# Optimization experiments

Hardware: AMD Instinct MI355X
Metric: run time of the kernel (lower is better)

Reference implementation:

```python
import jax, jax.numpy as jnp
import numpy as np
from jax import lax

N, C, S_CH = 16, 256, 512  # batch, content channels (c_in=c_out), style channels
DN = ('NCHW', 'OIHW', 'NCHW')


def setup_inputs() -> dict:
    key = jax.random.key(0)
    ks = jax.random.split(key, 8)
    p = lambda k, s: jax.random.normal(k, s, jnp.float32) * 0.05
    return {
        'style_encoding': jax.random.normal(ks[0], (N, S_CH, 4, 4), jnp.float32),
        'content_in': jax.random.normal(ks[1], (N, C, 64, 64), jnp.float32),
        # depthwise_kernel_conv: Conv2d(512, n_groups=1, kernel=2)
        'dw_w': p(ks[2], (1, S_CH, 2, 2)), 'dw_b': p(ks[3], (1,)),
        # pw_cn_kn: Conv2d(512, pointwise_groups=1, 1)
        'pw_kn_w': p(ks[4], (1, S_CH, 1, 1)), 'pw_kn_b': p(ks[5], (1,)),
        # pw_cn_bias: Conv2d(512, c_out=256, 1)
        'pw_bias_w': p(ks[6], (C, S_CH, 1, 1)), 'pw_bias_b': p(ks[7], (C,)),
    }


def reference(style_encoding, content_in, dw_w, dw_b, pw_kn_w, pw_kn_b, pw_bias_w, pw_bias_b):
    n = style_encoding.shape[0]
    # depthwise kernel prediction: (N,1,3,3) -> expand -> (N, c_out, c_in, 3, 3)
    dk = lax.conv_general_dilated(style_encoding, dw_w, (1, 1), 'VALID',
                                  dimension_numbers=DN) + dw_b[None, :, None, None]
    depthwise = jnp.broadcast_to(dk[:, None], (n, C, C, 3, 3))
    # AvgPool2d(4) on 4x4 spatial == global mean -> (N,512,1,1)
    s_d = jnp.mean(style_encoding, axis=(2, 3))  # (N,512)
    # 1x1 convs on 1x1 spatial are plain matmuls
    pw1 = s_d @ pw_kn_w[:, :, 0, 0].T + pw_kn_b              # (N,1)
    pointwise_kn = jnp.broadcast_to(pw1[:, None, :, None, None], (n, C, C, 1, 1))
    pointwise_bias = s_d @ pw_bias_w[:, :, 0, 0].T + pw_bias_b  # (N,256)
    # ReflectionPad2d((1,1,1,1))
    x = jnp.pad(content_in, ((0, 0), (0, 0), (1, 1), (1, 1)), mode='reflect')

    def sample_conv(xi, wi, pwi, bi):
        # xi: (C,H+2,W+2), wi: (C,C,3,3) dynamic per-sample weight (groups=1)
        d = lax.conv_general_dilated(xi[None], wi, (1, 1), 'VALID',
                                     dimension_numbers=DN)[0]  # (C,H,W)
        # pointwise 1x1 conv with per-sample weight + bias
        return jnp.einsum('oi,ihw->ohw', pwi[:, :, 0, 0], d) + bi[:, None, None]

    return jax.vmap(sample_conv)(x, depthwise, pointwise_kn, pointwise_bias)
```

## Files before the change

### kernel.cpp

```cpp
#include <hip/hip_runtime.h>


#define OFF_SCALE 0
#define OFF_K     16
#define OFF_SD    160
#define OFF_XP    8352

__global__ __launch_bounds__(256, 2) void ada_front(
    const float* __restrict__ style,
    const float* __restrict__ content,
    const float* __restrict__ dw_w,
    const float* __restrict__ dw_b,
    const float* __restrict__ pw_kn_w,
    const float* __restrict__ pw_kn_b,
    float* __restrict__ ws)
{
    const int t = threadIdx.x;
    __shared__ float red[4][10];

    if (blockIdx.x >= 16) {
        const int b  = blockIdx.x - 16;
        const int n  = b >> 5;
        const int g  = (b >> 2) & 7;
        const int pt = b & 3;
        const int p4 = pt * 256 + t;

        const float4* src = (const float4*)content
                          + ((size_t)(n * 256 + g * 32)) * 1024 + p4;
        float4 a = make_float4(0.f, 0.f, 0.f, 0.f);
#pragma unroll 8
        for (int c = 0; c < 32; ++c) {
            float4 v = src[(size_t)c * 1024];
            a.x += v.x; a.y += v.y; a.z += v.z; a.w += v.w;
        }
        ((float4*)(ws + OFF_XP))[((size_t)(n * 8 + g)) * 1024 + p4] = a;
        return;
    }

    const int n = blockIdx.x;

    float acc[10];
#pragma unroll
    for (int j = 0; j < 10; ++j) acc[j] = 0.f;

#pragma unroll
    for (int cc = 0; cc < 2; ++cc) {
        const int c = t + cc * 256;
        const float4* sp = (const float4*)(style + ((size_t)n * 512 + c) * 16);
        float v[16];
#pragma unroll
        for (int q = 0; q < 4; ++q) {
            float4 f = sp[q];
            v[q*4+0] = f.x; v[q*4+1] = f.y; v[q*4+2] = f.z; v[q*4+3] = f.w;
        }
        float sum = 0.f;
#pragma unroll
        for (int q = 0; q < 16; ++q) sum += v[q];
        const float sdc = sum * 0.0625f;
        ws[OFF_SD + n * 512 + c] = sdc;

        const float* w = dw_w + c * 4;
        const float w00 = w[0], w01 = w[1], w10 = w[2], w11 = w[3];
#pragma unroll
        for (int ki = 0; ki < 3; ++ki)
#pragma unroll
            for (int kj = 0; kj < 3; ++kj)
                acc[ki*3+kj] += v[ki*4 + kj]       * w00
                              + v[ki*4 + kj + 1]   * w01
                              + v[(ki+1)*4 + kj]   * w10
                              + v[(ki+1)*4 + kj+1] * w11;
        acc[9] += sdc * pw_kn_w[c];
    }

#pragma unroll
    for (int off = 32; off >= 1; off >>= 1)
#pragma unroll
        for (int j = 0; j < 10; ++j)
            acc[j] += __shfl_down(acc[j], off, 64);

    if ((t & 63) == 0) {
#pragma unroll
        for (int j = 0; j < 10; ++j) red[t >> 6][j] = acc[j];
    }
    __syncthreads();

    if (t < 10) {
        const float s = red[0][t] + red[1][t] + red[2][t] + red[3][t];
        if (t < 9) ws[OFF_K + n * 9 + t] = s + dw_b[0];
        else       ws[OFF_SCALE + n]     = 256.f * (s + pw_kn_b[0]);
    }
}

__global__ __launch_bounds__(256, 2) void ada_back(
    const float* __restrict__ ws,
    const float* __restrict__ pw_bias_w,
    const float* __restrict__ pw_bias_b,
    float4* __restrict__ out)
{
    const int bid = blockIdx.x;
    const int n   = bid >> 6;
    const int s   = bid & 63;
    const int t   = threadIdx.x;

    __shared__ float Xs[4096];
    __shared__ float bias_s[4];

    {
        const int wv = t >> 6, l = t & 63;
        const int o  = s * 4 + wv;
        const float4* wr = (const float4*)(pw_bias_w + (size_t)o * 512);
        const float4* sv = (const float4*)(ws + OFF_SD + (size_t)n * 512);
        const float4 a0 = wr[l * 2],     a1 = wr[l * 2 + 1];
        const float4 s0 = sv[l * 2],     s1 = sv[l * 2 + 1];
        float d = a0.x*s0.x + a0.y*s0.y + a0.z*s0.z + a0.w*s0.w
                + a1.x*s1.x + a1.y*s1.y + a1.z*s1.z + a1.w*s1.w;
#pragma unroll
        for (int off = 32; off >= 1; off >>= 1)
            d += __shfl_down(d, off, 64);
        if (l == 0) bias_s[wv] = d + pw_bias_b[o];
    }

    const float4* Xp = (const float4*)(ws + OFF_XP) + (size_t)n * 8 * 1024;
#pragma unroll
    for (int i = 0; i < 4; ++i) {
        const int p4 = i * 256 + t;
        float4 a = Xp[p4];
#pragma unroll
        for (int g = 1; g < 8; ++g) {
            float4 v = Xp[g * 1024 + p4];
            a.x += v.x; a.y += v.y; a.z += v.z; a.w += v.w;
        }
        ((float4*)Xs)[p4] = a;
    }

    float k[9];
#pragma unroll
    for (int j = 0; j < 9; ++j) k[j] = ws[OFF_K + n * 9 + j];
    const float scale = ws[OFF_SCALE + n];
    __syncthreads();

    const float b0 = bias_s[0], b1 = bias_s[1], b2 = bias_s[2], b3 = bias_s[3];
    float4* obase = out + ((size_t)(n * 256 + s * 4)) * 1024;

#pragma unroll
    for (int q = 0; q < 4; ++q) {
        const int h  = q * 16 + (t >> 4);
        const int w0 = (t & 15) * 4;
        const int hm = (h == 0)  ? 1  : h - 1;
        const int hp = (h == 63) ? 62 : h + 1;
        float e0 = 0.f, e1 = 0.f, e2 = 0.f, e3 = 0.f;
        const int rows[3] = { hm, h, hp };
#pragma unroll
        for (int i = 0; i < 3; ++i) {
            const float* R = &Xs[rows[i] * 64];
            const float4 m    = *(const float4*)&R[w0];
            const float  left  = (w0 == 0)  ? R[1]  : R[w0 - 1];
            const float  right = (w0 == 60) ? R[62] : R[w0 + 4];
            const float k0 = k[i*3], k1 = k[i*3+1], k2 = k[i*3+2];
            e0 += k0*left + k1*m.x + k2*m.y;
            e1 += k0*m.x  + k1*m.y + k2*m.z;
            e2 += k0*m.y  + k1*m.z + k2*m.w;
            e3 += k0*m.z  + k1*m.w + k2*right;
        }
        e0 *= scale; e1 *= scale; e2 *= scale; e3 *= scale;

        float4* o = obase + q * 256 + t;
        o[0]    = make_float4(e0 + b0, e1 + b0, e2 + b0, e3 + b0);
        o[1024] = make_float4(e0 + b1, e1 + b1, e2 + b1, e3 + b1);
        o[2048] = make_float4(e0 + b2, e1 + b2, e2 + b2, e3 + b2);
        o[3072] = make_float4(e0 + b3, e1 + b3, e2 + b3, e3 + b3);
    }
}

extern "C" void kernel_launch(void* const* d_in, const int* in_sizes, int n_in,
                              void* d_out, int out_size, void* d_ws, size_t ws_size,
                              hipStream_t stream)
{
    const float* style     = (const float*)d_in[0];
    const float* content   = (const float*)d_in[1];
    const float* dw_w      = (const float*)d_in[2];
    const float* dw_b      = (const float*)d_in[3];
    const float* pw_kn_w   = (const float*)d_in[4];
    const float* pw_kn_b   = (const float*)d_in[5];
    const float* pw_bias_w = (const float*)d_in[6];
    const float* pw_bias_b = (const float*)d_in[7];
    float*  ws  = (float*)d_ws;
    float4* out = (float4*)d_out;

    ada_front<<<16 + 512, 256, 0, stream>>>(style, content, dw_w, dw_b,
                                            pw_kn_w, pw_kn_b, ws);
    ada_back <<<1024,     256, 0, stream>>>(ws, pw_bias_w, pw_bias_b, out);
}
```

Before: 31.03 us.

## Reduce all channel partials in front kernel via shared memory instead of back kernel

The front kernel's content-sum blocks now each cover a 32-float4 pixel slice across all 8 channel groups. They combine the 8 partial sums with a shared-memory tree reduction and write one fully reduced channel-sum per pixel. The back kernel then loads a single summed plane instead of reading and adding 8 partial planes in each of its 1024 blocks. This removes 8x redundant workspace reads per sample (64 blocks per sample each reread them). The cost is narrower per-block memory access (32 float4 per row segment) and extra barriers in the front kernel.

```diff
diff --git a/kernel.cpp b/kernel.cpp
--- a/kernel.cpp
+++ b/kernel.cpp
@@ -4,7 +4,7 @@
 #define OFF_SCALE 0
 #define OFF_K     16
 #define OFF_SD    160
-#define OFF_XP    8352
+#define OFF_XS    8352
 
 __global__ __launch_bounds__(256, 2) void ada_front(
     const float* __restrict__ style,
@@ -17,23 +17,40 @@
 {
     const int t = threadIdx.x;
     __shared__ float red[4][10];
+    __shared__ float4 part[8][32];
 
     if (blockIdx.x >= 16) {
-        const int b  = blockIdx.x - 16;
-        const int n  = b >> 5;
-        const int g  = (b >> 2) & 7;
-        const int pt = b & 3;
-        const int p4 = pt * 256 + t;
+        const int b   = blockIdx.x - 16;
+        const int n   = b >> 5;
+        const int sl  = b & 31;
+        const int col = t & 31;
+        const int g   = t >> 5;
 
         const float4* src = (const float4*)content
-                          + ((size_t)(n * 256 + g * 32)) * 1024 + p4;
+                          + ((size_t)(n * 256 + g * 32)) * 1024 + sl * 32 + col;
         float4 a = make_float4(0.f, 0.f, 0.f, 0.f);
 #pragma unroll 8
         for (int c = 0; c < 32; ++c) {
             float4 v = src[(size_t)c * 1024];
             a.x += v.x; a.y += v.y; a.z += v.z; a.w += v.w;
         }
-        ((float4*)(ws + OFF_XP))[((size_t)(n * 8 + g)) * 1024 + p4] = a;
+        part[g][col] = a;
+        __syncthreads();
+        if (g < 4) {
+            float4 v = part[g + 4][col], u = part[g][col];
+            part[g][col] = make_float4(u.x + v.x, u.y + v.y, u.z + v.z, u.w + v.w);
+        }
+        __syncthreads();
+        if (g < 2) {
+            float4 v = part[g + 2][col], u = part[g][col];
+            part[g][col] = make_float4(u.x + v.x, u.y + v.y, u.z + v.z, u.w + v.w);
+        }
+        __syncthreads();
+        if (g == 0) {
+            float4 v = part[1][col], u = part[0][col];
+            ((float4*)(ws + OFF_XS))[(size_t)n * 1024 + sl * 32 + col] =
+                make_float4(u.x + v.x, u.y + v.y, u.z + v.z, u.w + v.w);
+        }
         return;
     }
 
@@ -120,18 +137,10 @@
         if (l == 0) bias_s[wv] = d + pw_bias_b[o];
     }
 
-    const float4* Xp = (const float4*)(ws + OFF_XP) + (size_t)n * 8 * 1024;
-#pragma unroll
-    for (int i = 0; i < 4; ++i) {
-        const int p4 = i * 256 + t;
-        float4 a = Xp[p4];
-#pragma unroll
-        for (int g = 1; g < 8; ++g) {
-            float4 v = Xp[g * 1024 + p4];
-            a.x += v.x; a.y += v.y; a.z += v.z; a.w += v.w;
-        }
-        ((float4*)Xs)[p4] = a;
-    }
+    const float4* xg = (const float4*)(ws + OFF_XS) + (size_t)n * 1024;
+#pragma unroll
+    for (int i = 0; i < 4; ++i)
+        ((float4*)Xs)[i * 256 + t] = xg[i * 256 + t];
 
     float k[9];
 #pragma unroll
```

Measured after the change: 29.98 us. 3.4% less time.
